# Performance work log

Hardware: AMD Instinct MI355X
Metric: run time of the kernel (lower is better)

The kernel has to match this reference:

```python
import jax, jax.numpy as jnp
import numpy as np
from jax import lax

EPS = 1e-5
HALF = 32
LEVELS = 17  # 16-level quantization of [0,1) -> round(x*255/16) in {0..16}


def setup_inputs() -> dict:
    key = jax.random.key(0)
    ks = jax.random.split(key, 48)
    r = lambda i, s: jax.random.normal(ks[i], s, jnp.float32) * 0.1
    inp = {
        'x': jax.random.uniform(ks[0], (4, 3, 256, 256), jnp.float32),
        # prepare: 1x1 conv (3->32), depthwise 1x1 (per-channel scale), BN, then repeat
        'w1': r(1, (32, 3)), 'b1': r(2, (32,)),
        'w2': 1.0 + r(3, (32,)), 'b2': r(4, (32,)),
        'bn1g': 1.0 + r(5, (32,)), 'bn1b': r(6, (32,)), 'bn1m': r(7, (32,)), 'bn1v': jnp.abs(1.0 + r(8, (32,))),
        'w3': r(9, (32, 32)), 'b3': r(10, (32,)),
        'w4': 1.0 + r(11, (32,)), 'b4': r(12, (32,)),
        'bn2g': 1.0 + r(13, (32,)), 'bn2b': r(14, (32,)), 'bn2m': r(15, (32,)), 'bn2v': jnp.abs(1.0 + r(16, (32,))),
        # downgrade SharedConv: one 3x3 kernel shared across all channels, stride 3, pad 1
        'scw': r(17, (1, 1, 3, 3)), 'scb': r(18, ()),
        # interpolate branch A: SharedConv 5x5 pad 2 + BN
        'iaw': r(19, (1, 1, 5, 5)), 'iabias': r(20, ()),
        'iabg': 1.0 + r(21, (32,)), 'iabb': r(22, (32,)), 'iabm': r(23, (32,)), 'iabv': jnp.abs(1.0 + r(24, (32,))),
        # interpolate branch B
        'ibw': r(25, (1, 1, 5, 5)), 'ibbias': r(26, ()),
        'ibbg': 1.0 + r(27, (32,)), 'ibbb': r(28, (32,)), 'ibbm': r(29, (32,)), 'ibbv': jnp.abs(1.0 + r(30, (32,))),
        'f1g': 1.0 + r(31, (64,)), 'f1b': r(32, (64,)), 'f1m': r(33, (64,)), 'f1v': jnp.abs(1.0 + r(34, (64,))),
        'f2g': 1.0 + r(35, (64,)), 'f2b': r(36, (64,)), 'f2m': r(37, (64,)), 'f2v': jnp.abs(1.0 + r(38, (64,))),
    }
    return inp


def _bn(x, g, b, m, v):
    # eval-mode BatchNorm2d with running stats; params broadcast over [B,C,H,W]
    return (x - m[:, None, None]) * (g[:, None, None] / jnp.sqrt(v[:, None, None] + EPS)) + b[:, None, None]


def _lrelu(x):
    return jnp.where(x >= 0, x, 0.01 * x)


def _mode_pool(x, k=11, stride=1, padding=1):
    # x is already quantized to levels q/16, q in {0..16}; pad with 0 (= level 0)
    x = jnp.pad(x, ((0, 0), (0, 0), (padding, padding), (padding, padding)))
    q = jnp.round(x * 16.0).astype(jnp.int32)  # [B,C,Hp,Wp] integer levels
    onehot = (q[None] == jnp.arange(LEVELS, dtype=jnp.int32)[:, None, None, None, None]).astype(jnp.float32)
    counts = lax.reduce_window(onehot, 0.0, lax.add, (1, 1, 1, k, k), (1, 1, 1, stride, stride), 'VALID')
    # argmax returns the FIRST max -> smallest modal value (torch.mode tie-break)
    return jnp.argmax(counts, axis=0).astype(jnp.float32) / 16.0


def _shared_conv(x, w, b, stride, padding):
    # single kxk kernel shared across all channels (depthwise with tied weight)
    B, C, H, W = x.shape
    y = lax.conv_general_dilated(x.reshape(B * C, 1, H, W), w, (stride, stride),
                                 ((padding, padding), (padding, padding)),
                                 dimension_numbers=('NCHW', 'OIHW', 'NCHW'))
    return y.reshape(B, C, y.shape[2], y.shape[3]) + b


def _ft(x, f1g, f1b, f1m, f1v, f2g, f2b, f2m, f2v):
    x = _bn(x, f1g, f1b, f1m, f1v)
    x = jnp.where(x > 0.1, x, 0.7 * x)  # MaxLeakyReLU(scale=0.7, threshold=0.1)
    x = _bn(x, f2g, f2b, f2m, f2v)
    # EmphaseLocal: gate by local contrast vs 11x11 mean (count_include_pad avg)
    xp = jnp.pad(x, ((0, 0), (0, 0), (5, 5), (5, 5)))
    mean = lax.reduce_window(xp, 0.0, lax.add, (1, 1, 11, 11), (1, 1, 1, 1), 'VALID') / 121.0
    return x * jax.nn.sigmoid(x - mean)


def reference(x, w1, b1, w2, b2, bn1g, bn1b, bn1m, bn1v, w3, b3, w4, b4, bn2g, bn2b, bn2m, bn2v,
              scw, scb, iaw, iabias, iabg, iabb, iabm, iabv, ibw, ibbias, ibbg, ibbb, ibbm, ibbv,
              f1g, f1b, f1m, f1v, f2g, f2b, f2m, f2v):
    B, C, H, W = x.shape
    # prepare: ColorDownsample(16) -> ModePool2d(11,1,1) -> 1x1 conv -> dw 1x1 -> BN -> LReLU (x2)
    d = jnp.round(x * 255.0 / 16.0) * 16.0 / 256.0
    d = _mode_pool(d)
    d = jnp.einsum('bchw,oc->bohw', d, w1) + b1[:, None, None]
    d = d * w2[:, None, None] + b2[:, None, None]
    d = _lrelu(_bn(d, bn1g, bn1b, bn1m, bn1v))
    d = jnp.einsum('bchw,oc->bohw', d, w3) + b3[:, None, None]
    d = d * w4[:, None, None] + b4[:, None, None]
    d = _lrelu(_bn(d, bn2g, bn2b, bn2m, bn2v))

    n = int(np.floor(np.log(min(d.shape[2], d.shape[3])) / np.log(3)))
    score = jnp.zeros((B, 2 * HALF, H, W), jnp.float32)
    for _ in range(n):
        d = _shared_conv(d, scw, scb, 3, 1)  # downgrade
        z = jax.image.resize(d, (B, HALF, H, W), 'bilinear')
        a = _lrelu(_bn(_shared_conv(z, iaw, iabias, 1, 2), iabg, iabb, iabm, iabv))
        bch = _lrelu(_bn(_shared_conv(z, ibw, ibbias, 1, 2), ibbg, ibbb, ibbm, ibbv))
        score = score + jnp.concatenate([a, bch], axis=1)  # Splitter + Stack(1)

    for _ in range(3):
        score = _ft(score, f1g, f1b, f1m, f1v, f2g, f2b, f2m, f2v)
    return score / n
```

## Files before the change

kernel.cpp:

```cpp
#include <hip/hip_runtime.h>
#include <math.h>

#define EPSI 1e-5f

#define P_D1 2048
#define P_D2 (P_D1 + 128*83*83)
#define P_D3 (P_D2 + 128*28*28)
#define P_D4 (P_D3 + 128*10*10)
#define P_D5 (P_D4 + 128*4*4)
#define P_SCORE (P_D5 + 128*2*2)
#define P_D  P_SCORE
#define P_TAB (P_SCORE + 8388608)

__device__ __forceinline__ float rfl(float x) {
  return __builtin_bit_cast(float, __builtin_amdgcn_readfirstlane(__builtin_bit_cast(int, x)));
}

struct PrepArgs { const float* p[39]; };

__global__ void k_prep(PrepArgs a, float* __restrict__ P) {
  int t = threadIdx.x;
  const float *w1=a.p[1],*b1=a.p[2],*w2=a.p[3],*b2=a.p[4],*g1=a.p[5],*bb1=a.p[6],*m1=a.p[7],*v1=a.p[8];
  const float *w3=a.p[9],*b3=a.p[10],*w4=a.p[11],*b4=a.p[12],*g2=a.p[13],*bb2=a.p[14],*m2=a.p[15],*v2=a.p[16];
  for (int i=t;i<96;i+=256){ int o=i/3; float s=g1[o]/sqrtf(v1[o]+EPSI); P[i]=w1[i]*w2[o]*s; }
  for (int o=t;o<32;o+=256){ float s=g1[o]/sqrtf(v1[o]+EPSI); P[96+o]=(b1[o]*w2[o]+b2[o]-m1[o])*s+bb1[o]; }
  for (int i=t;i<1024;i+=256){ int o2=i/32; float s=g2[o2]/sqrtf(v2[o2]+EPSI); P[128+i]=w3[i]*w4[o2]*s; }
  for (int o=t;o<32;o+=256){ float s=g2[o]/sqrtf(v2[o]+EPSI); P[1152+o]=(b3[o]*w4[o]+b4[o]-m2[o])*s+bb2[o]; }
  const float *iag=a.p[21],*iab=a.p[22],*iam=a.p[23],*iav=a.p[24],*iabias=a.p[20];
  for (int c=t;c<32;c+=256){ float s=iag[c]/sqrtf(iav[c]+EPSI); P[1184+c]=s; P[1216+c]=(iabias[0]-iam[c])*s+iab[c]; }
  const float *ibg=a.p[27],*ibb=a.p[28],*ibm=a.p[29],*ibv=a.p[30],*ibbias=a.p[26];
  for (int c=t;c<32;c+=256){ float s=ibg[c]/sqrtf(ibv[c]+EPSI); P[1248+c]=s; P[1280+c]=(ibbias[0]-ibm[c])*s+ibb[c]; }
  const float *f1g=a.p[31],*f1b=a.p[32],*f1m=a.p[33],*f1v=a.p[34];
  for (int c=t;c<64;c+=256){ float s=f1g[c]/sqrtf(f1v[c]+EPSI); P[1312+c]=s; P[1376+c]=f1b[c]-f1m[c]*s; }
  const float *f2g=a.p[35],*f2b=a.p[36],*f2m=a.p[37],*f2v=a.p[38];
  for (int c=t;c<64;c+=256){ float s=f2g[c]/sqrtf(f2v[c]+EPSI); P[1440+c]=s; P[1504+c]=f2b[c]-f2m[c]*s; }
}

__global__ __launch_bounds__(256) void k_table(const float* __restrict__ P, float* __restrict__ T) {
  int idx = blockIdx.x*256 + threadIdx.x;
  if (idx >= 4913) return;
  int m0 = idx/289; int rem = idx - m0*289; int m1 = rem/17; int m2 = rem - m1*17;
  float md0 = (float)m0*0.0625f, md1 = (float)m1*0.0625f, md2 = (float)m2*0.0625f;
  const float* A1 = P;           const float* C1 = P + 96;
  const float* A2 = P + 128;     const float* C2 = P + 1152;
  float h[32];
  #pragma unroll
  for (int o = 0; o < 32; o++) {
    float v = C1[o] + A1[o*3]*md0 + A1[o*3+1]*md1 + A1[o*3+2]*md2;
    h[o] = (v >= 0.f) ? v : 0.01f*v;
  }
  float* tp = T + (size_t)idx*32;
  #pragma unroll
  for (int o2 = 0; o2 < 32; o2++) {
    float acc = C2[o2];
    #pragma unroll
    for (int o = 0; o < 32; o++) acc += A2[o2*32+o]*h[o];
    tp[o2] = (acc >= 0.f) ? acc : 0.01f*acc;
  }
}

__global__ __launch_bounds__(256) void k_mode_mlp(const float* __restrict__ x,
                                                 const float* __restrict__ T,
                                                 float* __restrict__ dout) {
  __shared__ int qs[3*676];
  __shared__ unsigned CH[3*1326];
  int lx = threadIdx.x, ly = threadIdx.y;
  int tid = ly*16 + lx;
  int tx0 = blockIdx.x*16, ty0 = blockIdx.y*16;
  int b = blockIdx.z;
  for (int k = tid; k < 3*676; k += 256) {
    int cch = k/676; int rem = k - cch*676; int r = rem/26; int cc = rem - r*26;
    int gy = ty0 + r - 1, gx = tx0 + cc - 1;
    int q = 0;
    if ((unsigned)gy < 256u && (unsigned)gx < 256u) {
      float v = x[((size_t)(b*3+cch)*256 + gy)*256 + gx];
      q = (int)rintf(v*255.0f/16.0f);
      q = q < 0 ? 0 : (q > 16 ? 16 : q);
    }
    qs[k] = q;
  }
  __syncthreads();

  if (tid < 156) {
    int half = tid & 1; int rem = tid >> 1;
    int cx = rem % 26; int ch = rem / 26;
    const int* qp = &qs[ch*676 + cx];
    int oy0 = half*8;
    unsigned w0=0, w1=0, w2=0;
    #pragma unroll 1
    for (int r = oy0; r < oy0+11; r++) {
      int q = qp[r*26];
      unsigned inc = 1u << ((q & 7) << 2);
      int sel = q >> 3;
      w0 += (sel==0)?inc:0u; w1 += (sel==1)?inc:0u; w2 += (sel==2)?inc:0u;
    }
    unsigned base = (unsigned)(ch*442 + cx*17 + oy0);
    CH[base] = w0; CH[1326+base] = w1; CH[2652+base] = w2;
    #pragma unroll 1
    for (int i = 1; i < 8; i++) {
      int qr = qp[(oy0+i-1)*26];
      unsigned incr = 1u << ((qr & 7) << 2);
      int selr = qr >> 3;
      w0 -= (selr==0)?incr:0u; w1 -= (selr==1)?incr:0u; w2 -= (selr==2)?incr:0u;
      int qa = qp[(oy0+i+10)*26];
      unsigned inca = 1u << ((qa & 7) << 2);
      int sela = qa >> 3;
      w0 += (sela==0)?inca:0u; w1 += (sela==1)?inca:0u; w2 += (sela==2)?inca:0u;
      CH[base+i] = w0; CH[1326+base+i] = w1; CH[2652+base+i] = w2;
    }
  }
  __syncthreads();

  int oi = ty0 + ly, oj = tx0 + lx;
  if (oi >= 248 || oj >= 248) return;

  int mode[3];
  #pragma unroll
  for (int ch = 0; ch < 3; ch++) {
    unsigned a0=0,a1=0,a2=0,a3=0,a4=0;
    unsigned base = (unsigned)(ch*442 + lx*17 + ly);
    #pragma unroll
    for (int d = 0; d < 11; d++) {
      unsigned r0 = CH[base + d*17];
      unsigned r1 = CH[1326 + base + d*17];
      unsigned r2 = CH[2652 + base + d*17];
      a0 += r0 & 0x0F0F0F0Fu;
      a1 += (r0 >> 4) & 0x0F0F0F0Fu;
      a2 += r1 & 0x0F0F0F0Fu;
      a3 += (r1 >> 4) & 0x0F0F0F0Fu;
      a4 += r2;
    }
    int best = -1, m = 0;
    #define CHK2(l, w) { int cnt = (int)(((w) >> ((((l)>>1)&3)*8)) & 255u); if (cnt > best) { best = cnt; m = (l); } }
    CHK2(0,a0) CHK2(1,a1) CHK2(2,a0) CHK2(3,a1) CHK2(4,a0) CHK2(5,a1) CHK2(6,a0) CHK2(7,a1)
    CHK2(8,a2) CHK2(9,a3) CHK2(10,a2) CHK2(11,a3) CHK2(12,a2) CHK2(13,a3) CHK2(14,a2) CHK2(15,a3)
    { int cnt = (int)(a4 & 255u); if (cnt > best) { best = cnt; m = 16; } }
    #undef CHK2
    mode[ch] = m;
  }
  int idx = (mode[0]*17 + mode[1])*17 + mode[2];
  const float* tp = T + (size_t)idx*32;
  size_t ob = ((size_t)(b*32)*248 + oi)*248 + oj;
  #pragma unroll
  for (int o2 = 0; o2 < 32; o2 += 4) {
    float4 v = *(const float4*)(tp + o2);
    dout[ob + (size_t)o2*61504]     = v.x;
    dout[ob + (size_t)(o2+1)*61504] = v.y;
    dout[ob + (size_t)(o2+2)*61504] = v.z;
    dout[ob + (size_t)(o2+3)*61504] = v.w;
  }
}

__global__ void k_down(const float* __restrict__ in, float* __restrict__ out,
                       const float* __restrict__ scw, const float* __restrict__ scb) {
  const int Hin = 248, Hout = 83, total = 128*83*83;
  int idx = blockIdx.x*256 + threadIdx.x;
  if (idx >= total) return;
  float w[9];
  #pragma unroll
  for (int i = 0; i < 9; i++) w[i] = rfl(scw[i]);
  float bias = rfl(scb[0]);
  int j = idx % Hout; int t2 = idx / Hout; int i = t2 % Hout; int p = t2 / Hout;
  const float* base = in + (size_t)p*Hin*Hin;
  float s = bias;
  #pragma unroll
  for (int u = 0; u < 3; u++) {
    int r = 3*i - 1 + u;
    if ((unsigned)r < (unsigned)Hin) {
      #pragma unroll
      for (int v = 0; v < 3; v++) {
        int cc = 3*j - 1 + v;
        if ((unsigned)cc < (unsigned)Hin) s += base[(size_t)r*Hin + cc]*w[u*3+v];
      }
    }
  }
  out[idx] = s;
}

__global__ __launch_bounds__(256) void k_down_rest(const float* __restrict__ in, float* __restrict__ ws,
                                                   const float* __restrict__ scw, const float* __restrict__ scb) {
  __shared__ float buf[6889 + 784 + 100 + 16];
  int tid = threadIdx.x; int p = blockIdx.x;
  float w[9];
  #pragma unroll
  for (int i = 0; i < 9; i++) w[i] = rfl(scw[i]);
  float bias = rfl(scb[0]);
  const float* src = in + (size_t)p*6889;
  for (int k = tid; k < 6889; k += 256) buf[k] = src[k];
  __syncthreads();
  const int HIN[4] = {83,28,10,4}, HOUT[4] = {28,10,4,2};
  const int OIN[4] = {0, 6889, 6889+784, 6889+784+100};
  const size_t GOFF[4] = {P_D2, P_D3, P_D4, P_D5};
  #pragma unroll
  for (int st = 0; st < 4; st++) {
    const int hin = HIN[st], hout = HOUT[st];
    const float* bi = buf + OIN[st];
    float* bo = buf + OIN[st] + hin*hin;
    float* go = ws + GOFF[st] + (size_t)p*(hout*hout);
    for (int k = tid; k < hout*hout; k += 256) {
      int i = k/hout, j = k - i*hout;
      float s = bias;
      #pragma unroll
      for (int u = 0; u < 3; u++) {
        int r = 3*i - 1 + u;
        if ((unsigned)r < (unsigned)hin) {
          #pragma unroll
          for (int v = 0; v < 3; v++) {
            int cc = 3*j - 1 + v;
            if ((unsigned)cc < (unsigned)hin) s += bi[r*hin + cc]*w[u*3+v];
          }
        }
      }
      bo[k] = s; go[k] = s;
    }
    __syncthreads();
  }
}

#define NSP_PACK (83u | (28u<<7) | (10u<<14) | (4u<<21) | (2u<<28))
#define ZROT(r) ((((r)&3) ^ (((r)>>2)&3)) << 3)
__global__ __launch_bounds__(256) void k_accum(const float* __restrict__ ws,
                                               const float* __restrict__ iaw,
                                               const float* __restrict__ ibw,
                                               float* __restrict__ score) {
  __shared__ __align__(16) float hrow[14*96];
  __shared__ __align__(16) float zt[36*96];
  int tid = threadIdx.x;
  int c = blockIdx.y, b = blockIdx.z;
  int tx0 = (blockIdx.x & 3)*64, ty0 = (blockIdx.x >> 2)*32;
  int half = tid >> 7;
  int t2 = tid & 127;
  int lx4 = (t2 & 15)*4, lyt = t2 >> 4;

  const float* wp = half ? ibw : iaw;
  float w[25];
  #pragma unroll
  for (int i = 0; i < 25; i++) w[i] = rfl(wp[i]);
  float s_ = rfl(ws[1184 + half*64 + c]);
  float C_ = rfl(ws[1216 + half*64 + c]);

  int bzy = tid >> 3;
  int bzx0 = tid & 7;

  float acc[16];
  #pragma unroll
  for (int i = 0; i < 16; i++) acc[i] = 0.f;

  size_t off = P_D1;
  #pragma unroll 1
  for (int lvl = 0; lvl < 5; lvl++) {
    const int n = (int)((NSP_PACK >> (7*lvl)) & 127u);
    const float inv = (float)n * (1.f/256.f);
    float f0 = ((float)(ty0-2)+0.5f)*inv - 0.5f;
    float f1 = ((float)(ty0+33)+0.5f)*inv - 0.5f;
    int yb0 = min(max((int)floorf(f0),0), n-2);
    int yb1 = min(max((int)floorf(f1),0), n-2);
    int rows = yb1 - yb0 + 2;
    const float* dp = ws + off + (size_t)(b*32+c)*(n*n);

    #pragma unroll 1
    for (int k = tid; k < rows*68; k += 256) {
      int r = k/68, zx = k - r*68;
      int gx = tx0 + zx - 2;
      float h = 0.f;
      if ((unsigned)gx < 256u) {
        float f = ((float)gx + 0.5f)*inv - 0.5f;
        float ff = floorf(f);
        int i0 = (int)ff;
        int xb = min(max(i0,0), n-2);
        float wx = (i0 < 0) ? 0.f : (i0 > n-2 ? 1.f : f - ff);
        const float* rp = dp + (yb0 + r)*n + xb;
        h = rp[0] + wx*(rp[1] - rp[0]);
      }
      hrow[r*96 + ((r&3)<<3) + zx] = h;
    }
    __syncthreads();

    {
      int gy = ty0 - 2 + bzy;
      float f = ((float)gy + 0.5f)*inv - 0.5f;
      float ff = floorf(f);
      int i0 = (int)ff;
      int yb = min(max(i0,0), n-2);
      float wy = (i0 < 0) ? 0.f : (i0 > n-2 ? 1.f : f - ff);
      bool vy = ((unsigned)gy < 256u);
      int rel = yb - yb0;
      int ra = rel*96 + ((rel&3)<<3);
      int rb = (rel+1)*96 + (((rel+1)&3)<<3);
      int zr0 = bzy*96 + ZROT(bzy);
      #pragma unroll
      for (int s = 0; s < 9; s++) {
        int zx = bzx0 + s*8;
        if (zx < 68) {
          float v = 0.f;
          if (vy) { float a = hrow[ra + zx], bb = hrow[rb + zx]; v = a + wy*(bb - a); }
          zt[zr0 + zx] = v;
        }
      }
      #pragma unroll 1
      for (int k = tid; k < 4*68; k += 256) {
        int zy = 32 + k/68; int zx = k - (k/68)*68;
        int gy2 = ty0 - 2 + zy;
        float v = 0.f;
        if ((unsigned)gy2 < 256u) {
          float f2 = ((float)gy2 + 0.5f)*inv - 0.5f;
          float ff2 = floorf(f2);
          int i02 = (int)ff2;
          int yb2 = min(max(i02,0), n-2);
          float wy2 = (i02 < 0) ? 0.f : (i02 > n-2 ? 1.f : f2 - ff2);
          int rel2 = yb2 - yb0;
          float a = hrow[rel2*96 + ((rel2&3)<<3) + zx];
          float bb = hrow[(rel2+1)*96 + (((rel2+1)&3)<<3) + zx];
          v = a + wy2*(bb - a);
        }
        zt[zy*96 + ZROT(zy) + zx] = v;
      }
    }
    __syncthreads();

    float cc[4][4];
    #pragma unroll
    for (int p = 0; p < 4; p++)
      #pragma unroll
      for (int j = 0; j < 4; j++) cc[p][j] = 0.f;
    #pragma unroll
    for (int zr = 0; zr < 8; zr++) {
      int row = 4*lyt + zr;
      int o = row*96 + ZROT(row) + lx4;
      float4 a0 = *(const float4*)&zt[o];
      float4 a1 = *(const float4*)&zt[o+4];
      float zz[8] = {a0.x,a0.y,a0.z,a0.w,a1.x,a1.y,a1.z,a1.w};
      #pragma unroll
      for (int p = 0; p < 4; p++) {
        int r = zr - p;
        if (r >= 0 && r < 5) {
          #pragma unroll
          for (int j = 0; j < 4; j++)
            #pragma unroll
            for (int v = 0; v < 5; v++)
              cc[p][j] += zz[j+v]*w[r*5+v];
        }
      }
    }
    #pragma unroll
    for (int p = 0; p < 4; p++)
      #pragma unroll
      for (int j = 0; j < 4; j++) {
        float v = cc[p][j]*s_ + C_;
        acc[p*4+j] += (v >= 0.f) ? v : 0.01f*v;
      }
    off += (size_t)128*n*n;
  }
  int oy = ty0 + 4*lyt, ox = tx0 + lx4;
  size_t base = ((size_t)(b*64 + half*32 + c)*256 + oy)*256 + ox;
  #pragma unroll
  for (int p = 0; p < 4; p++)
    *(float4*)&score[base + (size_t)p*256] = make_float4(acc[p*4],acc[p*4+1],acc[p*4+2],acc[p*4+3]);
}

__global__ __launch_bounds__(256) void k_ft(const float* __restrict__ in,
                                            float* __restrict__ out,
                                            const float* __restrict__ P, float scale) {
  __shared__ float Bf[16*271];
  int tid = threadIdx.x;
  int c = blockIdx.y, b = blockIdx.z;
  int ty0 = blockIdx.x * 16;
  float fs1 = rfl(P[1312+c]), fc1 = rfl(P[1376+c]), fs2 = rfl(P[1440+c]), fc2 = rfl(P[1504+c]);
  const float* ip = in + (size_t)(b*64 + c)*65536 + tid;

  if (tid < 160) {
    int r = tid / 10, q = tid - r*10;
    Bf[r*271 + (q < 5 ? q : 256 + q)] = 0.f;
  }

  float yreg[16];
  float win[11];
  float run = 0.f;
  #pragma unroll
  for (int s = 0; s < 26; s++) {
    int gy = ty0 + s - 5;
    float yv = 0.f;
    if ((unsigned)gy < 256u) {
      float t = ip[(size_t)gy*256]*fs1 + fc1;
      t = (t > 0.1f) ? t : 0.7f*t;
      yv = t*fs2 + fc2;
    }
    win[s % 11] = yv;
    run += yv;
    if (s >= 5 && s <= 20) yreg[s-5] = yv;
    if (s >= 10) {
      Bf[(s-10)*271 + 5 + tid] = run;
      run -= win[(s-10) % 11];
    }
  }
  __syncthreads();

  const size_t ob = (size_t)(b*64 + c)*65536 + (size_t)ty0*256 + tid;
  #pragma unroll
  for (int r = 0; r < 16; r++) {
    const float* bfr = Bf + r*271 + tid;
    float s = bfr[0];
    #pragma unroll
    for (int d = 1; d < 11; d++) s += bfr[d];
    float y = yreg[r];
    float sig = 1.f/(1.f + __expf(-(y - s*(1.f/121.f))));
    out[ob + (size_t)r*256] = y*sig*scale;
  }
}

extern "C" void kernel_launch(void* const* d_in, const int* in_sizes, int n_in,
                              void* d_out, int out_size, void* d_ws, size_t ws_size,
                              hipStream_t stream) {
  const float* x = (const float*)d_in[0];
  float* ws = (float*)d_ws;
  float* out = (float*)d_out;

  PrepArgs pa;
  for (int i = 0; i < 39; i++) pa.p[i] = (const float*)d_in[i];
  k_prep<<<dim3(1), dim3(256), 0, stream>>>(pa, ws);
  k_table<<<dim3(20), dim3(256), 0, stream>>>(ws, ws + P_TAB);

  k_mode_mlp<<<dim3(16,16,4), dim3(16,16), 0, stream>>>(x, ws + P_TAB, ws + P_D);

  const float* scw = (const float*)d_in[17];
  const float* scb = (const float*)d_in[18];
  {
    int total = 128*83*83;
    k_down<<<dim3((total+255)/256), dim3(256), 0, stream>>>(ws + P_D, ws + P_D1, scw, scb);
  }
  k_down_rest<<<dim3(128), dim3(256), 0, stream>>>(ws + P_D1, ws, scw, scb);

  k_accum<<<dim3(32,32,4), dim3(256), 0, stream>>>(ws, (const float*)d_in[19],
                                                   (const float*)d_in[25], ws + P_SCORE);

  k_ft<<<dim3(16,64,4), dim3(256), 0, stream>>>(ws + P_SCORE, out, ws, 1.f);
  k_ft<<<dim3(16,64,4), dim3(256), 0, stream>>>(out, ws + P_SCORE, ws, 1.f);
  k_ft<<<dim3(16,64,4), dim3(256), 0, stream>>>(ws + P_SCORE, out, ws, 0.2f);
}
```

Before: 371.9 us.

## Fuse param prep into table kernel, branchless mode argmax, packed FMA in accum

Merges the parameter-folding kernel into the table kernel. Each block recomputes the folded parameters into shared memory, and block 0 writes them back to global for later kernels, which removes one launch. The mode-pool argmax becomes a branchless max over packed count/level keys, with ties broken toward the lower level. The 5x5 conv accumulation in k_accum uses two-wide float vectors so the compiler can emit packed FMAs. The cost is redundant parameter folding in every table block.

```diff
diff --git a/kernel.cpp b/kernel.cpp
--- a/kernel.cpp
+++ b/kernel.cpp
@@ -2,6 +2,8 @@
 #include <math.h>
 
 #define EPSI 1e-5f
+
+typedef float f32x2 __attribute__((ext_vector_type(2)));
 
 #define P_D1 2048
 #define P_D2 (P_D1 + 128*83*83)
@@ -18,31 +20,36 @@
 
 struct PrepArgs { const float* p[39]; };
 
-__global__ void k_prep(PrepArgs a, float* __restrict__ P) {
+__global__ __launch_bounds__(256) void k_table(PrepArgs a, float* __restrict__ P,
+                                               float* __restrict__ T) {
+  __shared__ float Pl[1568];
   int t = threadIdx.x;
-  const float *w1=a.p[1],*b1=a.p[2],*w2=a.p[3],*b2=a.p[4],*g1=a.p[5],*bb1=a.p[6],*m1=a.p[7],*v1=a.p[8];
-  const float *w3=a.p[9],*b3=a.p[10],*w4=a.p[11],*b4=a.p[12],*g2=a.p[13],*bb2=a.p[14],*m2=a.p[15],*v2=a.p[16];
-  for (int i=t;i<96;i+=256){ int o=i/3; float s=g1[o]/sqrtf(v1[o]+EPSI); P[i]=w1[i]*w2[o]*s; }
-  for (int o=t;o<32;o+=256){ float s=g1[o]/sqrtf(v1[o]+EPSI); P[96+o]=(b1[o]*w2[o]+b2[o]-m1[o])*s+bb1[o]; }
-  for (int i=t;i<1024;i+=256){ int o2=i/32; float s=g2[o2]/sqrtf(v2[o2]+EPSI); P[128+i]=w3[i]*w4[o2]*s; }
-  for (int o=t;o<32;o+=256){ float s=g2[o]/sqrtf(v2[o]+EPSI); P[1152+o]=(b3[o]*w4[o]+b4[o]-m2[o])*s+bb2[o]; }
-  const float *iag=a.p[21],*iab=a.p[22],*iam=a.p[23],*iav=a.p[24],*iabias=a.p[20];
-  for (int c=t;c<32;c+=256){ float s=iag[c]/sqrtf(iav[c]+EPSI); P[1184+c]=s; P[1216+c]=(iabias[0]-iam[c])*s+iab[c]; }
-  const float *ibg=a.p[27],*ibb=a.p[28],*ibm=a.p[29],*ibv=a.p[30],*ibbias=a.p[26];
-  for (int c=t;c<32;c+=256){ float s=ibg[c]/sqrtf(ibv[c]+EPSI); P[1248+c]=s; P[1280+c]=(ibbias[0]-ibm[c])*s+ibb[c]; }
-  const float *f1g=a.p[31],*f1b=a.p[32],*f1m=a.p[33],*f1v=a.p[34];
-  for (int c=t;c<64;c+=256){ float s=f1g[c]/sqrtf(f1v[c]+EPSI); P[1312+c]=s; P[1376+c]=f1b[c]-f1m[c]*s; }
-  const float *f2g=a.p[35],*f2b=a.p[36],*f2m=a.p[37],*f2v=a.p[38];
-  for (int c=t;c<64;c+=256){ float s=f2g[c]/sqrtf(f2v[c]+EPSI); P[1440+c]=s; P[1504+c]=f2b[c]-f2m[c]*s; }
-}
-
-__global__ __launch_bounds__(256) void k_table(const float* __restrict__ P, float* __restrict__ T) {
-  int idx = blockIdx.x*256 + threadIdx.x;
+  {
+    const float *w1=a.p[1],*b1=a.p[2],*w2=a.p[3],*b2=a.p[4],*g1=a.p[5],*bb1=a.p[6],*m1=a.p[7],*v1=a.p[8];
+    const float *w3=a.p[9],*b3=a.p[10],*w4=a.p[11],*b4=a.p[12],*g2=a.p[13],*bb2=a.p[14],*m2=a.p[15],*v2=a.p[16];
+    for (int i=t;i<96;i+=256){ int o=i/3; float s=g1[o]/sqrtf(v1[o]+EPSI); Pl[i]=w1[i]*w2[o]*s; }
+    for (int o=t;o<32;o+=256){ float s=g1[o]/sqrtf(v1[o]+EPSI); Pl[96+o]=(b1[o]*w2[o]+b2[o]-m1[o])*s+bb1[o]; }
+    for (int i=t;i<1024;i+=256){ int o2=i/32; float s=g2[o2]/sqrtf(v2[o2]+EPSI); Pl[128+i]=w3[i]*w4[o2]*s; }
+    for (int o=t;o<32;o+=256){ float s=g2[o]/sqrtf(v2[o]+EPSI); Pl[1152+o]=(b3[o]*w4[o]+b4[o]-m2[o])*s+bb2[o]; }
+    const float *iag=a.p[21],*iab=a.p[22],*iam=a.p[23],*iav=a.p[24],*iabias=a.p[20];
+    for (int c=t;c<32;c+=256){ float s=iag[c]/sqrtf(iav[c]+EPSI); Pl[1184+c]=s; Pl[1216+c]=(iabias[0]-iam[c])*s+iab[c]; }
+    const float *ibg=a.p[27],*ibb=a.p[28],*ibm=a.p[29],*ibv=a.p[30],*ibbias=a.p[26];
+    for (int c=t;c<32;c+=256){ float s=ibg[c]/sqrtf(ibv[c]+EPSI); Pl[1248+c]=s; Pl[1280+c]=(ibbias[0]-ibm[c])*s+ibb[c]; }
+    const float *f1g=a.p[31],*f1b=a.p[32],*f1m=a.p[33],*f1v=a.p[34];
+    for (int c=t;c<64;c+=256){ float s=f1g[c]/sqrtf(f1v[c]+EPSI); Pl[1312+c]=s; Pl[1376+c]=f1b[c]-f1m[c]*s; }
+    const float *f2g=a.p[35],*f2b=a.p[36],*f2m=a.p[37],*f2v=a.p[38];
+    for (int c=t;c<64;c+=256){ float s=f2g[c]/sqrtf(f2v[c]+EPSI); Pl[1440+c]=s; Pl[1504+c]=f2b[c]-f2m[c]*s; }
+  }
+  __syncthreads();
+  if (blockIdx.x == 0) {
+    for (int i = t; i < 1568; i += 256) P[i] = Pl[i];
+  }
+  int idx = blockIdx.x*256 + t;
   if (idx >= 4913) return;
   int m0 = idx/289; int rem = idx - m0*289; int m1 = rem/17; int m2 = rem - m1*17;
   float md0 = (float)m0*0.0625f, md1 = (float)m1*0.0625f, md2 = (float)m2*0.0625f;
-  const float* A1 = P;           const float* C1 = P + 96;
-  const float* A2 = P + 128;     const float* C2 = P + 1152;
+  const float* A1 = Pl;           const float* C1 = Pl + 96;
+  const float* A2 = Pl + 128;     const float* C2 = Pl + 1152;
   float h[32];
   #pragma unroll
   for (int o = 0; o < 32; o++) {
@@ -130,13 +137,15 @@
       a3 += (r1 >> 4) & 0x0F0F0F0Fu;
       a4 += r2;
     }
-    int best = -1, m = 0;
-    #define CHK2(l, w) { int cnt = (int)(((w) >> ((((l)>>1)&3)*8)) & 255u); if (cnt > best) { best = cnt; m = (l); } }
-    CHK2(0,a0) CHK2(1,a1) CHK2(2,a0) CHK2(3,a1) CHK2(4,a0) CHK2(5,a1) CHK2(6,a0) CHK2(7,a1)
-    CHK2(8,a2) CHK2(9,a3) CHK2(10,a2) CHK2(11,a3) CHK2(12,a2) CHK2(13,a3) CHK2(14,a2) CHK2(15,a3)
-    { int cnt = (int)(a4 & 255u); if (cnt > best) { best = cnt; m = 16; } }
-    #undef CHK2
-    mode[ch] = m;
+    unsigned best = 0u;
+    #define KEY(l, wreg) { unsigned cnt = ((wreg) >> ((((l)>>1)&3)*8)) & 255u; \
+                           unsigned key = cnt*32u + (31u - (unsigned)(l)); \
+                           best = (key > best) ? key : best; }
+    KEY(0,a0) KEY(1,a1) KEY(2,a0) KEY(3,a1) KEY(4,a0) KEY(5,a1) KEY(6,a0) KEY(7,a1)
+    KEY(8,a2) KEY(9,a3) KEY(10,a2) KEY(11,a3) KEY(12,a2) KEY(13,a3) KEY(14,a2) KEY(15,a3)
+    { unsigned cnt = a4 & 255u; unsigned key = cnt*32u + 15u; best = (key > best) ? key : best; }
+    #undef KEY
+    mode[ch] = 31 - (int)(best & 31u);
   }
   int idx = (mode[0]*17 + mode[1])*17 + mode[2];
   const float* tp = T + (size_t)idx*32;
@@ -318,11 +327,11 @@
     }
     __syncthreads();
 
-    float cc[4][4];
+    f32x2 cc2[4][2];
     #pragma unroll
     for (int p = 0; p < 4; p++)
       #pragma unroll
-      for (int j = 0; j < 4; j++) cc[p][j] = 0.f;
+      for (int j2 = 0; j2 < 2; j2++) cc2[p][j2] = (f32x2)(0.f);
     #pragma unroll
     for (int zr = 0; zr < 8; zr++) {
       int row = 4*lyt + zr;
@@ -335,19 +344,24 @@
         int r = zr - p;
         if (r >= 0 && r < 5) {
           #pragma unroll
-          for (int j = 0; j < 4; j++)
-            #pragma unroll
-            for (int v = 0; v < 5; v++)
-              cc[p][j] += zz[j+v]*w[r*5+v];
+          for (int v = 0; v < 5; v++) {
+            float wv = w[r*5+v];
+            cc2[p][0] += (f32x2){zz[v],   zz[v+1]} * wv;
+            cc2[p][1] += (f32x2){zz[v+2], zz[v+3]} * wv;
+          }
         }
       }
     }
     #pragma unroll
     for (int p = 0; p < 4; p++)
       #pragma unroll
-      for (int j = 0; j < 4; j++) {
-        float v = cc[p][j]*s_ + C_;
-        acc[p*4+j] += (v >= 0.f) ? v : 0.01f*v;
+      for (int j2 = 0; j2 < 2; j2++) {
+        f32x2 v2 = cc2[p][j2]*s_ + C_;
+        #pragma unroll
+        for (int e = 0; e < 2; e++) {
+          float v = v2[e];
+          acc[p*4 + j2*2 + e] += (v >= 0.f) ? v : 0.01f*v;
+        }
       }
     off += (size_t)128*n*n;
   }
@@ -417,8 +431,7 @@
 
   PrepArgs pa;
   for (int i = 0; i < 39; i++) pa.p[i] = (const float*)d_in[i];
-  k_prep<<<dim3(1), dim3(256), 0, stream>>>(pa, ws);
-  k_table<<<dim3(20), dim3(256), 0, stream>>>(ws, ws + P_TAB);
+  k_table<<<dim3(20), dim3(256), 0, stream>>>(pa, ws, ws + P_TAB);
 
   k_mode_mlp<<<dim3(16,16,4), dim3(16,16), 0, stream>>>(x, ws + P_TAB, ws + P_D);
 
```

After: 361.2 us. 1.03x faster.
